# Kernel optimization log

Measured on AMD Instinct MI355X. Metric: run time of the kernel, lower is better.

The kernel has to match this reference:

```python
import jax, jax.numpy as jnp
import numpy as np

B = 32768      # number of sets
N = 131072     # total elements
DIM = 128      # feature dim
HID = 64       # hidden dim
MAXP = 17      # max_n + 1 (one-hot positional dim / size-class count)


def _ln(x, g, b, eps=1e-5):
    m = jnp.mean(x, -1, keepdims=True)
    v = jnp.var(x, -1, keepdims=True)
    return (x - m) * jax.lax.rsqrt(v + eps) * g + b


def _mlp_ln(x, w1, b1, g, bt, w2, b2):
    return jnp.tanh(_ln(x @ w1 + b1, g, bt)) @ w2 + b2


def _mlp(x, w1, b1, w2, b2):
    return jnp.tanh(x @ w1 + b1) @ w2 + b2


def _lin_init(key, fan_in, fan_out):
    k1, k2 = jax.random.split(key)
    s = 1.0 / np.sqrt(fan_in)
    return (jax.random.uniform(k1, (fan_in, fan_out), jnp.float32, -s, s),
            jax.random.uniform(k2, (fan_out,), jnp.float32, -s, s))


def setup_inputs() -> dict:
    key = jax.random.key(0)
    ks = jax.random.split(key, 16)
    inp = {}
    inp['x'] = jax.random.normal(ks[0], (N, DIM), jnp.float32)
    inp['batch'] = jnp.sort(jax.random.randint(ks[1], (N,), 0, B)).astype(jnp.int64)
    # rank: Linear(dim, 1)
    inp['rank_w'], inp['rank_b'] = _lin_init(ks[2], DIM, 1)
    # enc_psi: dim -> 96 -> hid, LayerNorm
    inp['psi_w1'], inp['psi_b1'] = _lin_init(ks[3], DIM, 96)
    inp['psi_g'] = jnp.ones((96,), jnp.float32); inp['psi_bt'] = jnp.zeros((96,), jnp.float32)
    inp['psi_w2'], inp['psi_b2'] = _lin_init(ks[4], 96, HID)
    # encoder pos_encoder: 17 -> 40 -> hid, LayerNorm
    inp['pe_e_w1'], inp['pe_e_b1'] = _lin_init(ks[5], MAXP, 40)
    inp['pe_e_g'] = jnp.ones((40,), jnp.float32); inp['pe_e_bt'] = jnp.zeros((40,), jnp.float32)
    inp['pe_e_w2'], inp['pe_e_b2'] = _lin_init(ks[6], 40, HID)
    # enc_phi: (hid+17)=81 -> 72 -> hid, no LN
    inp['phi_w1'], inp['phi_b1'] = _lin_init(ks[7], HID + MAXP, 72)
    inp['phi_w2'], inp['phi_b2'] = _lin_init(ks[8], 72, HID)
    # size_pred: hid -> 40 -> 17, no LN
    inp['size_w1'], inp['size_b1'] = _lin_init(ks[9], HID, 40)
    inp['size_w2'], inp['size_b2'] = _lin_init(ks[10], 40, MAXP)
    # decoder pos_encoder: 17 -> 40 -> hid, LayerNorm
    inp['pe_d_w1'], inp['pe_d_b1'] = _lin_init(ks[11], MAXP, 40)
    inp['pe_d_g'] = jnp.ones((40,), jnp.float32); inp['pe_d_bt'] = jnp.zeros((40,), jnp.float32)
    inp['pe_d_w2'], inp['pe_d_b2'] = _lin_init(ks[12], 40, HID)
    # decoder: hid -> 96 -> dim, no LN
    inp['dec_w1'], inp['dec_b1'] = _lin_init(ks[13], HID, 96)
    inp['dec_w2'], inp['dec_b2'] = _lin_init(ks[14], 96, DIM)
    return inp


def reference(x, batch, rank_w, rank_b,
              psi_w1, psi_b1, psi_g, psi_bt, psi_w2, psi_b2,
              pe_e_w1, pe_e_b1, pe_e_g, pe_e_bt, pe_e_w2, pe_e_b2,
              phi_w1, phi_b1, phi_w2, phi_b2,
              size_w1, size_b1, size_w2, size_b2,
              pe_d_w1, pe_d_b1, pe_d_g, pe_d_bt, pe_d_w2, pe_d_b2,
              dec_w1, dec_b1, dec_w2, dec_b2):
    batch = batch.astype(jnp.int32)
    # ---- Encoder ----
    n = jax.ops.segment_sum(jnp.ones(N, jnp.int32), batch, num_segments=B)  # [B]
    seg_start = jnp.cumsum(n) - n                                           # ptr[:-1]
    mag = (x @ rank_w + rank_b).reshape(-1)                                 # rank scores
    idx = jnp.lexsort((mag, batch))  # per-segment sort (batch is grouped/sorted)
    xs = x[idx]                                                             # [N, DIM]
    keys = jnp.arange(N) - seg_start[batch]                                 # position in set
    pos = jax.nn.one_hot(keys, MAXP, dtype=x.dtype)                         # [N, MAXP]
    y1 = _mlp_ln(xs, psi_w1, psi_b1, psi_g, psi_bt, psi_w2, psi_b2) * \
         _mlp_ln(pos, pe_e_w1, pe_e_b1, pe_e_g, pe_e_bt, pe_e_w2, pe_e_b2)
    y2 = jax.ops.segment_sum(y1, batch, num_segments=B)                     # [B, HID]
    pos_n = jax.nn.one_hot(n, MAXP, dtype=x.dtype)
    z = _mlp(jnp.concatenate([y2, pos_n], -1), phi_w1, phi_b1, phi_w2, phi_b2)  # [B, HID]
    # ---- Decoder ----
    logits = _mlp(z, size_w1, size_b1, size_w2, size_b2)                    # [B, MAXP]
    n_dec = jnp.argmax(logits, -1)                                          # [B]
    pe = _mlp_ln(jnp.eye(MAXP, dtype=x.dtype),
                 pe_d_w1, pe_d_b1, pe_d_g, pe_d_bt, pe_d_w2, pe_d_b2)       # [MAXP, HID]
    zp = z[:, None, :] * pe[None, :, :]                                     # [B, MAXP, HID]
    xr = _mlp(zp, dec_w1, dec_b1, dec_w2, dec_b2)                           # [B, MAXP, DIM]
    mask = jnp.arange(MAXP)[None, :] < n_dec[:, None]                       # valid slots
    xr = jnp.where(mask[..., None], xr, 0.0)
    batchr = jnp.broadcast_to(jnp.arange(B)[:, None], (B, MAXP))
    return xr.reshape(B * MAXP, DIM), batchr.reshape(-1), mask.reshape(-1)
```

## Files before the change

kernel.cpp:

```cpp
#include <hip/hip_runtime.h>

#define NELEM 131072
#define BSETS 32768
#define DIM 128
#define HID 64
#define MAXP 17

typedef __attribute__((ext_vector_type(8))) short short8;
typedef __attribute__((ext_vector_type(4))) float f32x4;

__device__ __forceinline__ unsigned short f2bf(float f) {
  unsigned u = __float_as_uint(f);
  u += 0x7fff + ((u >> 16) & 1);
  return (unsigned short)(u >> 16);
}

__global__ __launch_bounds__(256) void k_bounds(const int* __restrict__ batch,
                                                int* __restrict__ start) {
  int i = blockIdx.x * 256 + threadIdx.x;
  int b = batch[i];
  if (i == 0) {
    for (int bb = 0; bb <= b; ++bb) start[bb] = 0;
  } else {
    int bp = batch[i - 1];
    for (int bb = bp + 1; bb <= b; ++bb) start[bb] = i;
  }
  if (i == NELEM - 1) {
    for (int bb = b + 1; bb <= BSETS; ++bb) start[bb] = NELEM;
  }
}

__global__ __launch_bounds__(256) void k_mag(const float* __restrict__ x,
                                             const float* __restrict__ rank_w,
                                             const float* __restrict__ rank_b,
                                             double* __restrict__ mag) {
  int t = threadIdx.x;
  int lane = t & 63;
  int w = t >> 6;
  float2 wv = ((const float2*)rank_w)[lane];
  double w0 = wv.x, w1 = wv.y;
  double rb = rank_b[0];
  int rowbase = (blockIdx.x * 4 + w) * 32;
  for (int it = 0; it < 32; ++it) {
    int row = rowbase + it;
    float2 xv = ((const float2*)(x + (size_t)row * DIM))[lane];
    double acc = (double)xv.x * w0 + (double)xv.y * w1;
#pragma unroll
    for (int m = 1; m < 64; m <<= 1)
      acc += __shfl_xor(acc, m, 64);
    if (lane == 0) mag[row] = acc + rb;
  }
}

__global__ __launch_bounds__(256) void k_rank(const int* __restrict__ batch,
                                              const int* __restrict__ start,
                                              const double* __restrict__ mag,
                                              int* __restrict__ key) {
  int i = blockIdx.x * 256 + threadIdx.x;
  int b = batch[i];
  int s = start[b], e = start[b + 1];
  double mi = mag[i];
  int r = 0;
  for (int j = s; j < e; ++j) {
    double mj = mag[j];
    r += (mj < mi) || (mj == mi && j < i);
  }
  key[i] = r;
}

__device__ void pos_mlp40(int row, const float* w1, const float* b1, const float* g,
                          const float* bt, const float* w2, const float* b2, float* out) {
  float h[40];
  for (int j = 0; j < 40; ++j) h[j] = b1[j] + (row >= 0 ? w1[row * 40 + j] : 0.0f);
  float s = 0.f;
  for (int j = 0; j < 40; ++j) s += h[j];
  float mean = s * (1.0f / 40.0f);
  float v = 0.f;
  for (int j = 0; j < 40; ++j) { float d = h[j] - mean; v += d * d; }
  float rs = rsqrtf(v * (1.0f / 40.0f) + 1e-5f);
  float tb[40];
  for (int j = 0; j < 40; ++j) tb[j] = tanhf((h[j] - mean) * rs * g[j] + bt[j]);
  for (int o = 0; o < 64; ++o) {
    float a = b2[o];
    for (int j = 0; j < 40; ++j) a += tb[j] * w2[j * 64 + o];
    out[o] = a;
  }
}

__global__ void k_tables(const float* ew1, const float* eb1, const float* eg, const float* ebt,
                         const float* ew2, const float* eb2,
                         const float* dw1, const float* db1, const float* dg, const float* dbt,
                         const float* dw2, const float* db2,
                         float* enc_tab, float* dec_tab) {
  int t = threadIdx.x;
  if (t < 18) {
    float out[64];
    pos_mlp40(t < 17 ? t : -1, ew1, eb1, eg, ebt, ew2, eb2, out);
    for (int o = 0; o < 64; ++o) enc_tab[t * 64 + o] = out[o];
  } else if (t >= 32 && t < 49) {
    float out[64];
    pos_mlp40(t - 32, dw1, db1, dg, dbt, dw2, db2, out);
    for (int o = 0; o < 64; ++o) dec_tab[(t - 32) * 64 + o] = out[o];
  }
}

__global__ __launch_bounds__(256) void k_prep_w(const float* __restrict__ w1,
                                                const float* __restrict__ w2,
                                                unsigned short* __restrict__ w1s,
                                                unsigned short* __restrict__ w2s) {
  int idx = blockIdx.x * 256 + threadIdx.x;
  if (idx < 6144) {
    int i = idx & 7, lane = (idx >> 3) & 63, rest = idx >> 9;
    int jt = rest % 6, s = rest / 6;
    int k = s * 32 + (lane >> 4) * 8 + i;
    int n = jt * 16 + (lane & 15);
    w1s[idx] = f2bf(w1[k * 96 + n]);
  }
  int idx2 = idx - 6144;
  if (idx2 >= 0 && idx2 < 12288) {
    int i = idx2 & 7, lane = (idx2 >> 3) & 63, rest = idx2 >> 9;
    int jt = rest % 8, s = rest / 8;
    int k = s * 32 + (lane >> 4) * 8 + i;
    int n = jt * 16 + (lane & 15);
    w2s[idx2] = f2bf(w2[k * 128 + n]);
  }
}

__global__ __launch_bounds__(256) void k_encoder(
    const float* __restrict__ x, const int* __restrict__ batch,
    const int* __restrict__ key, const int* __restrict__ start,
    const float* __restrict__ w1, const float* __restrict__ b1,
    const float* __restrict__ g, const float* __restrict__ bt,
    const float* __restrict__ w2, const float* __restrict__ b2,
    const float* __restrict__ enc_tab, float* __restrict__ y1) {
  __shared__ float xt[64][129];
  __shared__ float tt[64][97];
  __shared__ float ps1[4][64];
  __shared__ float ps2[4][64];
  int t = threadIdx.x;
  int base = blockIdx.x * 64;
  const float4* xg = (const float4*)(x + (size_t)base * DIM);
#pragma unroll
  for (int v = 0; v < 8; ++v) {
    int f = t + 256 * v;
    float4 val = xg[f];
    int e = f >> 5, kq = (f & 31) * 4;
    xt[e][kq] = val.x; xt[e][kq + 1] = val.y; xt[e][kq + 2] = val.z; xt[e][kq + 3] = val.w;
  }
  __syncthreads();
  int lane = t & 63;
  int w = __builtin_amdgcn_readfirstlane(t >> 6);
  int j0 = w * 24;
  float acc[24];
#pragma unroll
  for (int jj = 0; jj < 24; ++jj) acc[jj] = b1[j0 + jj];
  for (int k = 0; k < DIM; ++k) {
    float xv = xt[lane][k];
#pragma unroll
    for (int jj = 0; jj < 24; ++jj) acc[jj] += xv * w1[k * 96 + j0 + jj];
  }
  float s1 = 0.f, s2 = 0.f;
#pragma unroll
  for (int jj = 0; jj < 24; ++jj) { s1 += acc[jj]; s2 += acc[jj] * acc[jj]; }
  ps1[w][lane] = s1; ps2[w][lane] = s2;
  __syncthreads();
  float S1 = ps1[0][lane] + ps1[1][lane] + ps1[2][lane] + ps1[3][lane];
  float S2 = ps2[0][lane] + ps2[1][lane] + ps2[2][lane] + ps2[3][lane];
  float mean = S1 * (1.0f / 96.0f);
  float var = S2 * (1.0f / 96.0f) - mean * mean;
  float rs = rsqrtf(var + 1e-5f);
#pragma unroll
  for (int jj = 0; jj < 24; ++jj) {
    float hv = (acc[jj] - mean) * rs * g[j0 + jj] + bt[j0 + jj];
    tt[lane][j0 + jj] = tanhf(hv);
  }
  __syncthreads();
  int o0 = w * 16;
  float acc2[16];
#pragma unroll
  for (int oo = 0; oo < 16; ++oo) acc2[oo] = b2[o0 + oo];
  for (int j = 0; j < 96; ++j) {
    float tv = tt[lane][j];
#pragma unroll
    for (int oo = 0; oo < 16; ++oo) acc2[oo] += tv * w2[j * 64 + o0 + oo];
  }
  int gi = base + lane;
  int kk = key[gi];
  int row = kk < MAXP ? kk : MAXP;
  int bb = batch[gi];
  int pos = start[bb] + kk;
  const float* pe = enc_tab + row * 64;
#pragma unroll
  for (int oo = 0; oo < 16; ++oo) acc2[oo] *= pe[o0 + oo];
  float4* d4 = (float4*)(y1 + (size_t)pos * 64 + o0);
#pragma unroll
  for (int q = 0; q < 4; ++q)
    d4[q] = make_float4(acc2[4 * q], acc2[4 * q + 1], acc2[4 * q + 2], acc2[4 * q + 3]);
}

__global__ __launch_bounds__(256) void k_segsum(const float* __restrict__ y1,
                                                const int* __restrict__ start,
                                                float* __restrict__ y2) {
  int idx = blockIdx.x * 256 + threadIdx.x;
  int b = idx >> 6, o = idx & 63;
  int s = start[b], e = start[b + 1];
  float acc = 0.f;
  for (int p = s; p < e; ++p) acc += y1[(size_t)p * 64 + o];
  y2[idx] = acc;
}

__global__ __launch_bounds__(256) void k_phi(const float* __restrict__ y2,
                                             const int* __restrict__ start,
                                             const float* __restrict__ w1, const float* __restrict__ b1,
                                             const float* __restrict__ w2, const float* __restrict__ b2,
                                             const float* __restrict__ sw1, const float* __restrict__ sb1,
                                             const float* __restrict__ sw2, const float* __restrict__ sb2,
                                             float* __restrict__ z, int* __restrict__ ndec) {
  __shared__ float yt[64][65];
  __shared__ float tt[64][73];
  __shared__ float zt[64][65];
  __shared__ float st[64][41];
  int t = threadIdx.x;
  int base = blockIdx.x * 64;
  const float4* yg = (const float4*)(y2 + (size_t)base * 64);
#pragma unroll
  for (int v = 0; v < 4; ++v) {
    int f = t + 256 * v;
    float4 val = yg[f];
    int e = f >> 4, kq = (f & 15) * 4;
    yt[e][kq] = val.x; yt[e][kq + 1] = val.y; yt[e][kq + 2] = val.z; yt[e][kq + 3] = val.w;
  }
  __syncthreads();
  int lane = t & 63;
  int w = __builtin_amdgcn_readfirstlane(t >> 6);
  int sb = base + lane;
  int nb = start[sb + 1] - start[sb];
  int j0 = w * 18;
  float acc[18];
#pragma unroll
  for (int jj = 0; jj < 18; ++jj) acc[jj] = b1[j0 + jj];
  for (int k = 0; k < 64; ++k) {
    float yv = yt[lane][k];
#pragma unroll
    for (int jj = 0; jj < 18; ++jj) acc[jj] += yv * w1[k * 72 + j0 + jj];
  }
  if (nb < MAXP) {
    const float* wr = w1 + (64 + nb) * 72 + j0;
#pragma unroll
    for (int jj = 0; jj < 18; ++jj) acc[jj] += wr[jj];
  }
#pragma unroll
  for (int jj = 0; jj < 18; ++jj) tt[lane][j0 + jj] = tanhf(acc[jj]);
  __syncthreads();
  int o0 = w * 16;
  float acc2[16];
#pragma unroll
  for (int oo = 0; oo < 16; ++oo) acc2[oo] = b2[o0 + oo];
  for (int j = 0; j < 72; ++j) {
    float tv = tt[lane][j];
#pragma unroll
    for (int oo = 0; oo < 16; ++oo) acc2[oo] += tv * w2[j * 64 + o0 + oo];
  }
  float4* zd = (float4*)(z + (size_t)sb * 64 + o0);
#pragma unroll
  for (int q = 0; q < 4; ++q)
    zd[q] = make_float4(acc2[4 * q], acc2[4 * q + 1], acc2[4 * q + 2], acc2[4 * q + 3]);
#pragma unroll
  for (int oo = 0; oo < 16; ++oo) zt[lane][o0 + oo] = acc2[oo];
  __syncthreads();
  int s0 = w * 10;
  float hs[10];
#pragma unroll
  for (int jj = 0; jj < 10; ++jj) hs[jj] = sb1[s0 + jj];
  for (int o = 0; o < 64; ++o) {
    float v = zt[lane][o];
#pragma unroll
    for (int jj = 0; jj < 10; ++jj) hs[jj] += v * sw1[o * 40 + s0 + jj];
  }
#pragma unroll
  for (int jj = 0; jj < 10; ++jj) st[lane][s0 + jj] = tanhf(hs[jj]);
  __syncthreads();
  if (w == 0) {
    float lg[17];
#pragma unroll
    for (int l = 0; l < 17; ++l) lg[l] = sb2[l];
    for (int j = 0; j < 40; ++j) {
      float tv = st[lane][j];
#pragma unroll
      for (int l = 0; l < 17; ++l) lg[l] += tv * sw2[j * 17 + l];
    }
    float best = lg[0]; int bi = 0;
#pragma unroll
    for (int l = 1; l < 17; ++l) if (lg[l] > best) { best = lg[l]; bi = l; }
    ndec[sb] = bi;
  }
}

__global__ __launch_bounds__(256) void k_decoder(
    const float* __restrict__ z, const float* __restrict__ dec_tab,
    const unsigned short* __restrict__ w1s, const unsigned short* __restrict__ w2s,
    const float* __restrict__ b1, const float* __restrict__ b2,
    const int* __restrict__ ndec, float* __restrict__ out0) {
  __shared__ __align__(16) unsigned short h2[64][104];
  int t = threadIdx.x;
  int lane = t & 63;
  int w = __builtin_amdgcn_readfirstlane(t >> 6);
  int quad = lane >> 4, m = lane & 15;
  int r = blockIdx.x * 64 + w * 16 + m;
  int b = r / 17, p = r - b * 17;
  const float* zr = z + (size_t)b * 64;
  const float* per = dec_tab + p * 64;
  short8 a1[2];
#pragma unroll
  for (int s = 0; s < 2; ++s) {
    int k0 = s * 32 + quad * 8;
#pragma unroll
    for (int i = 0; i < 8; ++i) {
      float v = zr[k0 + i] * per[k0 + i];
      ((unsigned short*)&a1[s])[i] = f2bf(v);
    }
  }
  const short8* w1f = (const short8*)w1s;
  f32x4 acc[6] = {};
#pragma unroll
  for (int jt = 0; jt < 6; ++jt) {
    acc[jt] = __builtin_amdgcn_mfma_f32_16x16x32_bf16(a1[0], w1f[jt * 64 + lane], acc[jt], 0, 0, 0);
    acc[jt] = __builtin_amdgcn_mfma_f32_16x16x32_bf16(a1[1], w1f[(6 + jt) * 64 + lane], acc[jt], 0, 0, 0);
  }
#pragma unroll
  for (int jt = 0; jt < 6; ++jt) {
    int col = jt * 16 + m;
    float bias = b1[col];
#pragma unroll
    for (int reg = 0; reg < 4; ++reg) {
      int rl = w * 16 + quad * 4 + reg;
      h2[rl][col] = f2bf(tanhf(acc[jt][reg] + bias));
    }
  }
  __syncthreads();
  short8 a2[3];
#pragma unroll
  for (int s = 0; s < 3; ++s)
    a2[s] = *(const short8*)&h2[w * 16 + m][s * 32 + quad * 8];
  const short8* w2f = (const short8*)w2s;
  f32x4 acc2[8] = {};
#pragma unroll
  for (int nt = 0; nt < 8; ++nt) {
#pragma unroll
    for (int s = 0; s < 3; ++s)
      acc2[nt] = __builtin_amdgcn_mfma_f32_16x16x32_bf16(a2[s], w2f[(s * 8 + nt) * 64 + lane], acc2[nt], 0, 0, 0);
  }
#pragma unroll
  for (int nt = 0; nt < 8; ++nt) {
    int n = nt * 16 + m;
    float bias = b2[n];
#pragma unroll
    for (int reg = 0; reg < 4; ++reg) {
      int rl = w * 16 + quad * 4 + reg;
      int rg = blockIdx.x * 64 + rl;
      int bb = rg / 17, pp = rg - bb * 17;
      float v = acc2[nt][reg] + bias;
      if (pp >= ndec[bb]) v = 0.0f;
      out0[(size_t)rg * 128 + n] = v;
    }
  }
}

__global__ __launch_bounds__(256) void k_outaux(const int* __restrict__ ndec,
                                                float* __restrict__ out1,
                                                float* __restrict__ out2) {
  int r = blockIdx.x * 256 + threadIdx.x;
  int b = r / 17, p = r - b * 17;
  out1[r] = (float)b;
  out2[r] = (p < ndec[b]) ? 1.0f : 0.0f;
}

extern "C" void kernel_launch(void* const* d_in, const int* in_sizes, int n_in,
                              void* d_out, int out_size, void* d_ws, size_t ws_size,
                              hipStream_t stream) {
  const float* x = (const float*)d_in[0];
  const int* batch = (const int*)d_in[1];
  const float* rank_w = (const float*)d_in[2];
  const float* rank_b = (const float*)d_in[3];
  const float* psi_w1 = (const float*)d_in[4];
  const float* psi_b1 = (const float*)d_in[5];
  const float* psi_g = (const float*)d_in[6];
  const float* psi_bt = (const float*)d_in[7];
  const float* psi_w2 = (const float*)d_in[8];
  const float* psi_b2 = (const float*)d_in[9];
  const float* pe_e_w1 = (const float*)d_in[10];
  const float* pe_e_b1 = (const float*)d_in[11];
  const float* pe_e_g = (const float*)d_in[12];
  const float* pe_e_bt = (const float*)d_in[13];
  const float* pe_e_w2 = (const float*)d_in[14];
  const float* pe_e_b2 = (const float*)d_in[15];
  const float* phi_w1 = (const float*)d_in[16];
  const float* phi_b1 = (const float*)d_in[17];
  const float* phi_w2 = (const float*)d_in[18];
  const float* phi_b2 = (const float*)d_in[19];
  const float* size_w1 = (const float*)d_in[20];
  const float* size_b1 = (const float*)d_in[21];
  const float* size_w2 = (const float*)d_in[22];
  const float* size_b2 = (const float*)d_in[23];
  const float* pe_d_w1 = (const float*)d_in[24];
  const float* pe_d_b1 = (const float*)d_in[25];
  const float* pe_d_g = (const float*)d_in[26];
  const float* pe_d_bt = (const float*)d_in[27];
  const float* pe_d_w2 = (const float*)d_in[28];
  const float* pe_d_b2 = (const float*)d_in[29];
  const float* dec_w1 = (const float*)d_in[30];
  const float* dec_b1 = (const float*)d_in[31];
  const float* dec_w2 = (const float*)d_in[32];
  const float* dec_b2 = (const float*)d_in[33];

  char* ws = (char*)d_ws;
  int* start = (int*)(ws);
  double* mag = (double*)(ws + 0x40000);
  int* key = (int*)(ws + 0x140000);
  float* enc_tab = (float*)(ws + 0x1C0000);
  float* dec_tab = (float*)(ws + 0x1C2000);
  unsigned short* w1s = (unsigned short*)(ws + 0x1C4000);
  unsigned short* w2s = (unsigned short*)(ws + 0x1C8000);
  float* zbuf = (float*)(ws + 0x200000);
  int* ndec = (int*)(ws + 0xA00000);

  float* out0 = (float*)d_out;
  float* out1 = out0 + 71303168;
  float* out2 = out1 + 557056;

  float* y1 = out0;
  float* y2 = out0 + 8388608;

  k_bounds<<<512, 256, 0, stream>>>(batch, start);
  k_mag<<<1024, 256, 0, stream>>>(x, rank_w, rank_b, mag);
  k_rank<<<512, 256, 0, stream>>>(batch, start, mag, key);
  k_tables<<<1, 64, 0, stream>>>(pe_e_w1, pe_e_b1, pe_e_g, pe_e_bt, pe_e_w2, pe_e_b2,
                                 pe_d_w1, pe_d_b1, pe_d_g, pe_d_bt, pe_d_w2, pe_d_b2,
                                 enc_tab, dec_tab);
  k_prep_w<<<72, 256, 0, stream>>>(dec_w1, dec_w2, w1s, w2s);
  k_encoder<<<2048, 256, 0, stream>>>(x, batch, key, start, psi_w1, psi_b1, psi_g, psi_bt,
                                      psi_w2, psi_b2, enc_tab, y1);
  k_segsum<<<8192, 256, 0, stream>>>(y1, start, y2);
  k_phi<<<512, 256, 0, stream>>>(y2, start, phi_w1, phi_b1, phi_w2, phi_b2,
                                 size_w1, size_b1, size_w2, size_b2, zbuf, ndec);
  k_decoder<<<8704, 256, 0, stream>>>(zbuf, dec_tab, w1s, w2s, dec_b1, dec_b2, ndec, out0);
  k_outaux<<<2176, 256, 0, stream>>>(ndec, out1, out2);
}
```

Before: 689.3 us.

## Fuse init kernels, fold segment sum into phi, merge aux outputs into decoder

Merges the bounds, magnitude, position-table and weight-prep kernels into one multi-role init kernel. Moves the segment sum into the phi kernel so the y2 intermediate is never written or read back. Writes the aux outputs (set index and mask) from the decoder, which cuts the launch count from ten kernels to five. The phi kernel now does irregular per-set reductions with four threads per set, which may load-balance worse than the old flat segsum.

```diff
diff --git a/kernel.cpp b/kernel.cpp
--- a/kernel.cpp
+++ b/kernel.cpp
@@ -13,59 +13,6 @@
   unsigned u = __float_as_uint(f);
   u += 0x7fff + ((u >> 16) & 1);
   return (unsigned short)(u >> 16);
-}
-
-__global__ __launch_bounds__(256) void k_bounds(const int* __restrict__ batch,
-                                                int* __restrict__ start) {
-  int i = blockIdx.x * 256 + threadIdx.x;
-  int b = batch[i];
-  if (i == 0) {
-    for (int bb = 0; bb <= b; ++bb) start[bb] = 0;
-  } else {
-    int bp = batch[i - 1];
-    for (int bb = bp + 1; bb <= b; ++bb) start[bb] = i;
-  }
-  if (i == NELEM - 1) {
-    for (int bb = b + 1; bb <= BSETS; ++bb) start[bb] = NELEM;
-  }
-}
-
-__global__ __launch_bounds__(256) void k_mag(const float* __restrict__ x,
-                                             const float* __restrict__ rank_w,
-                                             const float* __restrict__ rank_b,
-                                             double* __restrict__ mag) {
-  int t = threadIdx.x;
-  int lane = t & 63;
-  int w = t >> 6;
-  float2 wv = ((const float2*)rank_w)[lane];
-  double w0 = wv.x, w1 = wv.y;
-  double rb = rank_b[0];
-  int rowbase = (blockIdx.x * 4 + w) * 32;
-  for (int it = 0; it < 32; ++it) {
-    int row = rowbase + it;
-    float2 xv = ((const float2*)(x + (size_t)row * DIM))[lane];
-    double acc = (double)xv.x * w0 + (double)xv.y * w1;
-#pragma unroll
-    for (int m = 1; m < 64; m <<= 1)
-      acc += __shfl_xor(acc, m, 64);
-    if (lane == 0) mag[row] = acc + rb;
-  }
-}
-
-__global__ __launch_bounds__(256) void k_rank(const int* __restrict__ batch,
-                                              const int* __restrict__ start,
-                                              const double* __restrict__ mag,
-                                              int* __restrict__ key) {
-  int i = blockIdx.x * 256 + threadIdx.x;
-  int b = batch[i];
-  int s = start[b], e = start[b + 1];
-  double mi = mag[i];
-  int r = 0;
-  for (int j = s; j < e; ++j) {
-    double mj = mag[j];
-    r += (mj < mi) || (mj == mi && j < i);
-  }
-  key[i] = r;
 }
 
 __device__ void pos_mlp40(int row, const float* w1, const float* b1, const float* g,
@@ -87,43 +34,91 @@
   }
 }
 
-__global__ void k_tables(const float* ew1, const float* eb1, const float* eg, const float* ebt,
-                         const float* ew2, const float* eb2,
-                         const float* dw1, const float* db1, const float* dg, const float* dbt,
-                         const float* dw2, const float* db2,
-                         float* enc_tab, float* dec_tab) {
+__global__ __launch_bounds__(256) void k_init(
+    const float* __restrict__ x, const int* __restrict__ batch,
+    const float* __restrict__ rank_w, const float* __restrict__ rank_b,
+    double* __restrict__ mag, int* __restrict__ start,
+    const float* ew1, const float* eb1, const float* eg, const float* ebt,
+    const float* ew2, const float* eb2,
+    const float* dw1, const float* db1, const float* dg, const float* dbt,
+    const float* dw2, const float* db2,
+    float* enc_tab, float* dec_tab,
+    const float* __restrict__ decw1, const float* __restrict__ decw2,
+    unsigned short* __restrict__ w1s, unsigned short* __restrict__ w2s) {
+  int blk = blockIdx.x;
   int t = threadIdx.x;
-  if (t < 18) {
-    float out[64];
-    pos_mlp40(t < 17 ? t : -1, ew1, eb1, eg, ebt, ew2, eb2, out);
-    for (int o = 0; o < 64; ++o) enc_tab[t * 64 + o] = out[o];
-  } else if (t >= 32 && t < 49) {
-    float out[64];
-    pos_mlp40(t - 32, dw1, db1, dg, dbt, dw2, db2, out);
-    for (int o = 0; o < 64; ++o) dec_tab[(t - 32) * 64 + o] = out[o];
-  }
-}
-
-__global__ __launch_bounds__(256) void k_prep_w(const float* __restrict__ w1,
-                                                const float* __restrict__ w2,
-                                                unsigned short* __restrict__ w1s,
-                                                unsigned short* __restrict__ w2s) {
-  int idx = blockIdx.x * 256 + threadIdx.x;
-  if (idx < 6144) {
-    int i = idx & 7, lane = (idx >> 3) & 63, rest = idx >> 9;
-    int jt = rest % 6, s = rest / 6;
-    int k = s * 32 + (lane >> 4) * 8 + i;
-    int n = jt * 16 + (lane & 15);
-    w1s[idx] = f2bf(w1[k * 96 + n]);
-  }
-  int idx2 = idx - 6144;
-  if (idx2 >= 0 && idx2 < 12288) {
-    int i = idx2 & 7, lane = (idx2 >> 3) & 63, rest = idx2 >> 9;
-    int jt = rest % 8, s = rest / 8;
-    int k = s * 32 + (lane >> 4) * 8 + i;
-    int n = jt * 16 + (lane & 15);
-    w2s[idx2] = f2bf(w2[k * 128 + n]);
-  }
+  if (blk < 1024) {
+    int lane = t & 63;
+    int w = t >> 6;
+    float2 wv = ((const float2*)rank_w)[lane];
+    double w0 = wv.x, w1 = wv.y;
+    double rb = rank_b[0];
+    int rowbase = (blk * 4 + w) * 32;
+    for (int it = 0; it < 32; ++it) {
+      int row = rowbase + it;
+      float2 xv = ((const float2*)(x + (size_t)row * DIM))[lane];
+      double acc = (double)xv.x * w0 + (double)xv.y * w1;
+#pragma unroll
+      for (int m = 1; m < 64; m <<= 1)
+        acc += __shfl_xor(acc, m, 64);
+      if (lane == 0) mag[row] = acc + rb;
+    }
+  } else if (blk < 1536) {
+    int i = (blk - 1024) * 256 + t;
+    int b = batch[i];
+    if (i == 0) {
+      for (int bb = 0; bb <= b; ++bb) start[bb] = 0;
+    } else {
+      int bp = batch[i - 1];
+      for (int bb = bp + 1; bb <= b; ++bb) start[bb] = i;
+    }
+    if (i == NELEM - 1) {
+      for (int bb = b + 1; bb <= BSETS; ++bb) start[bb] = NELEM;
+    }
+  } else if (blk == 1536) {
+    if (t < 18) {
+      float out[64];
+      pos_mlp40(t < 17 ? t : -1, ew1, eb1, eg, ebt, ew2, eb2, out);
+      for (int o = 0; o < 64; ++o) enc_tab[t * 64 + o] = out[o];
+    } else if (t >= 32 && t < 49) {
+      float out[64];
+      pos_mlp40(t - 32, dw1, db1, dg, dbt, dw2, db2, out);
+      for (int o = 0; o < 64; ++o) dec_tab[(t - 32) * 64 + o] = out[o];
+    }
+  } else {
+    int idx = (blk - 1537) * 256 + t;
+    if (idx < 6144) {
+      int i = idx & 7, lane = (idx >> 3) & 63, rest = idx >> 9;
+      int jt = rest % 6, s = rest / 6;
+      int k = s * 32 + (lane >> 4) * 8 + i;
+      int n = jt * 16 + (lane & 15);
+      w1s[idx] = f2bf(decw1[k * 96 + n]);
+    }
+    int idx2 = idx - 6144;
+    if (idx2 >= 0 && idx2 < 12288) {
+      int i = idx2 & 7, lane = (idx2 >> 3) & 63, rest = idx2 >> 9;
+      int jt = rest % 8, s = rest / 8;
+      int k = s * 32 + (lane >> 4) * 8 + i;
+      int n = jt * 16 + (lane & 15);
+      w2s[idx2] = f2bf(decw2[k * 128 + n]);
+    }
+  }
+}
+
+__global__ __launch_bounds__(256) void k_rank(const int* __restrict__ batch,
+                                              const int* __restrict__ start,
+                                              const double* __restrict__ mag,
+                                              int* __restrict__ key) {
+  int i = blockIdx.x * 256 + threadIdx.x;
+  int b = batch[i];
+  int s = start[b], e = start[b + 1];
+  double mi = mag[i];
+  int r = 0;
+  for (int j = s; j < e; ++j) {
+    double mj = mag[j];
+    r += (mj < mi) || (mj == mi && j < i);
+  }
+  key[i] = r;
 }
 
 __global__ __launch_bounds__(256) void k_encoder(
@@ -198,18 +193,7 @@
     d4[q] = make_float4(acc2[4 * q], acc2[4 * q + 1], acc2[4 * q + 2], acc2[4 * q + 3]);
 }
 
-__global__ __launch_bounds__(256) void k_segsum(const float* __restrict__ y1,
-                                                const int* __restrict__ start,
-                                                float* __restrict__ y2) {
-  int idx = blockIdx.x * 256 + threadIdx.x;
-  int b = idx >> 6, o = idx & 63;
-  int s = start[b], e = start[b + 1];
-  float acc = 0.f;
-  for (int p = s; p < e; ++p) acc += y1[(size_t)p * 64 + o];
-  y2[idx] = acc;
-}
-
-__global__ __launch_bounds__(256) void k_phi(const float* __restrict__ y2,
+__global__ __launch_bounds__(256) void k_phi(const float* __restrict__ y1,
                                              const int* __restrict__ start,
                                              const float* __restrict__ w1, const float* __restrict__ b1,
                                              const float* __restrict__ w2, const float* __restrict__ b2,
@@ -222,13 +206,23 @@
   __shared__ float st[64][41];
   int t = threadIdx.x;
   int base = blockIdx.x * 64;
-  const float4* yg = (const float4*)(y2 + (size_t)base * 64);
-#pragma unroll
-  for (int v = 0; v < 4; ++v) {
-    int f = t + 256 * v;
-    float4 val = yg[f];
-    int e = f >> 4, kq = (f & 15) * 4;
-    yt[e][kq] = val.x; yt[e][kq + 1] = val.y; yt[e][kq + 2] = val.z; yt[e][kq + 3] = val.w;
+  {
+    int s = t >> 2, c = t & 3;
+    int sb = base + s;
+    int ps = start[sb], pe = start[sb + 1];
+    float acc[16];
+#pragma unroll
+    for (int i = 0; i < 16; ++i) acc[i] = 0.f;
+    for (int p = ps; p < pe; ++p) {
+      const float4* row = (const float4*)(y1 + (size_t)p * 64 + c * 16);
+#pragma unroll
+      for (int q = 0; q < 4; ++q) {
+        float4 v = row[q];
+        acc[4 * q] += v.x; acc[4 * q + 1] += v.y; acc[4 * q + 2] += v.z; acc[4 * q + 3] += v.w;
+      }
+    }
+#pragma unroll
+    for (int i = 0; i < 16; ++i) yt[s][c * 16 + i] = acc[i];
   }
   __syncthreads();
   int lane = t & 63;
@@ -300,7 +294,8 @@
     const float* __restrict__ z, const float* __restrict__ dec_tab,
     const unsigned short* __restrict__ w1s, const unsigned short* __restrict__ w2s,
     const float* __restrict__ b1, const float* __restrict__ b2,
-    const int* __restrict__ ndec, float* __restrict__ out0) {
+    const int* __restrict__ ndec, float* __restrict__ out0,
+    float* __restrict__ out1, float* __restrict__ out2) {
   __shared__ __align__(16) unsigned short h2[64][104];
   int t = threadIdx.x;
   int lane = t & 63;
@@ -364,15 +359,12 @@
       out0[(size_t)rg * 128 + n] = v;
     }
   }
-}
-
-__global__ __launch_bounds__(256) void k_outaux(const int* __restrict__ ndec,
-                                                float* __restrict__ out1,
-                                                float* __restrict__ out2) {
-  int r = blockIdx.x * 256 + threadIdx.x;
-  int b = r / 17, p = r - b * 17;
-  out1[r] = (float)b;
-  out2[r] = (p < ndec[b]) ? 1.0f : 0.0f;
+  if (t < 64) {
+    int rg = blockIdx.x * 64 + t;
+    int bb = rg / 17, pp = rg - bb * 17;
+    out1[rg] = (float)bb;
+    out2[rg] = (pp < ndec[bb]) ? 1.0f : 0.0f;
+  }
 }
 
 extern "C" void kernel_launch(void* const* d_in, const int* in_sizes, int n_in,
@@ -429,20 +421,16 @@
   float* out2 = out1 + 557056;
 
   float* y1 = out0;
-  float* y2 = out0 + 8388608;
-
-  k_bounds<<<512, 256, 0, stream>>>(batch, start);
-  k_mag<<<1024, 256, 0, stream>>>(x, rank_w, rank_b, mag);
+
+  k_init<<<1609, 256, 0, stream>>>(x, batch, rank_w, rank_b, mag, start,
+                                   pe_e_w1, pe_e_b1, pe_e_g, pe_e_bt, pe_e_w2, pe_e_b2,
+                                   pe_d_w1, pe_d_b1, pe_d_g, pe_d_bt, pe_d_w2, pe_d_b2,
+                                   enc_tab, dec_tab, dec_w1, dec_w2, w1s, w2s);
   k_rank<<<512, 256, 0, stream>>>(batch, start, mag, key);
-  k_tables<<<1, 64, 0, stream>>>(pe_e_w1, pe_e_b1, pe_e_g, pe_e_bt, pe_e_w2, pe_e_b2,
-                                 pe_d_w1, pe_d_b1, pe_d_g, pe_d_bt, pe_d_w2, pe_d_b2,
-                                 enc_tab, dec_tab);
-  k_prep_w<<<72, 256, 0, stream>>>(dec_w1, dec_w2, w1s, w2s);
   k_encoder<<<2048, 256, 0, stream>>>(x, batch, key, start, psi_w1, psi_b1, psi_g, psi_bt,
                                       psi_w2, psi_b2, enc_tab, y1);
-  k_segsum<<<8192, 256, 0, stream>>>(y1, start, y2);
-  k_phi<<<512, 256, 0, stream>>>(y2, start, phi_w1, phi_b1, phi_w2, phi_b2,
+  k_phi<<<512, 256, 0, stream>>>(y1, start, phi_w1, phi_b1, phi_w2, phi_b2,
                                  size_w1, size_b1, size_w2, size_b2, zbuf, ndec);
-  k_decoder<<<8704, 256, 0, stream>>>(zbuf, dec_tab, w1s, w2s, dec_b1, dec_b2, ndec, out0);
-  k_outaux<<<2176, 256, 0, stream>>>(ndec, out1, out2);
-}
+  k_decoder<<<8704, 256, 0, stream>>>(zbuf, dec_tab, w1s, w2s, dec_b1, dec_b2, ndec,
+                                      out0, out1, out2);
+}
```

After: 642.9 us. 1.07x faster.
